# Kernel optimization log

Measured on AMD Instinct MI355X. Metric: run time of the kernel, lower is better.

The kernel has to match this reference:

```python
import jax, jax.numpy as jnp
import numpy as np

B, N, VD, AD, SD, HD = 32, 2048, 512, 128, 128, 64

def _lin_params(key, out_d, in_d, scale=0.05):
    k1, k2 = jax.random.split(key)
    w = jax.random.normal(k1, (out_d, in_d), jnp.float32) * scale
    b = jax.random.normal(k2, (out_d,), jnp.float32) * scale
    return w, b

def setup_inputs() -> dict:
    key = jax.random.key(0)
    ks = jax.random.split(key, 10)
    inp = {
        'vfeat': jax.random.normal(ks[0], (B, N, VD), jnp.float32),
        'afeat': jax.random.normal(ks[1], (B, N, AD), jnp.float32),
    }
    inp['vfc_w'], inp['vfc_b'] = _lin_params(ks[2], SD, VD)
    inp['afc_w'], inp['afc_b'] = _lin_params(ks[3], SD, AD)
    inp['am_w'],  inp['am_b']  = _lin_params(ks[4], SD, SD)
    inp['U_w'],   inp['U_b']   = _lin_params(ks[5], HD, SD)
    inp['V_w'],   inp['V_b']   = _lin_params(ks[6], HD, SD)
    inp['W_w'],   inp['W_b']   = _lin_params(ks[7], 1, HD)
    inp['cls_w'], inp['cls_b'] = _lin_params(ks[8], 2, SD)
    return inp

def reference(vfeat, afeat, vfc_w, vfc_b, afc_w, afc_b, am_w, am_b,
              U_w, U_b, V_w, V_b, W_w, W_b, cls_w, cls_b):
    # eval mode: dropout = identity, no softmax on scores
    vo1 = jax.nn.relu(jnp.einsum('bnd,kd->bnk', vfeat, vfc_w) + vfc_b)   # [B,N,128]
    ax = jax.nn.relu(jnp.einsum('bnd,kd->bnk', afeat, afc_w) + afc_b)    # [B,N,128]
    # AM (gated cross-modal attention): attfeat = vo1 * sigmoid(Linear(ax))
    gate = jax.nn.sigmoid(jnp.einsum('bnk,jk->bnj', ax, am_w) + am_b)
    ffeat = vo1 * gate + vo1                                             # attfeat + vo1
    # gated attention score head
    v = jax.nn.relu(jnp.einsum('bnk,hk->bnh', ffeat, V_w) + V_b)
    u = jax.nn.sigmoid(jnp.einsum('bnk,hk->bnh', ffeat, U_w) + U_b)
    scores = jnp.einsum('bnh,oh->bno', v * u, W_w) + W_b                 # [B,N,1]
    s = scores[..., 0]                                                   # [B,N]
    # attention-weighted pooling (batched mm replaces per-sample loop)
    zfeat = jnp.einsum('bn,bnk->bk', s, ffeat)                           # [B,128]
    logits = jnp.einsum('bk,ck->bc', zfeat, cls_w) + cls_b               # [B,2]
    return (s, logits)
```

## Files before the change

kernel.cpp:

```cpp
#include <hip/hip_runtime.h>
#include <hip/hip_bf16.h>

#define B_   32
#define N_   2048
#define VD_  512
#define AD_  128
#define SD_  128
#define TM   128
#define THREADS 512

typedef __attribute__((ext_vector_type(8))) short short8;
typedef __attribute__((ext_vector_type(4))) float f32x4;

__device__ __forceinline__ float sigmoidf_(float x) { return 1.0f / (1.0f + __expf(-x)); }

__device__ __forceinline__ ushort f2bf(float x) {
    union { float f; unsigned int i; } v; v.f = x;
    unsigned int r = v.i + 0x7FFFu + ((v.i >> 16) & 1u);
    return (ushort)(r >> 16);
}
__device__ __forceinline__ float bf2f(ushort u) {
    union { unsigned int i; float f; } v; v.i = ((unsigned int)u) << 16; return v.f;
}

__device__ __forceinline__ int swz(int row, int k, int ldk) {
    return row * ldk + (k ^ ((row & 7) << 3));
}

__device__ __forceinline__ void gemm_chunk(const ushort* Ab, int ldkA, int kA0,
                                           const ushort* Wb,
                                           int wr, int wc, int t16, int g4,
                                           f32x4 (&acc)[2][4])
{
    #pragma unroll
    for (int kk = 0; kk < 2; ++kk) {
        const int k = kk * 32 + g4 * 8;
        short8 a0 = *(const short8*)&Ab[swz(32 * wr + t16,      kA0 + k, ldkA)];
        short8 a1 = *(const short8*)&Ab[swz(32 * wr + 16 + t16, kA0 + k, ldkA)];
        #pragma unroll
        for (int n = 0; n < 4; ++n) {
            short8 bf = *(const short8*)&Wb[swz(64 * wc + 16 * n + t16, k, 64)];
            acc[0][n] = __builtin_amdgcn_mfma_f32_16x16x32_bf16(a0, bf, acc[0][n], 0, 0, 0);
            acc[1][n] = __builtin_amdgcn_mfma_f32_16x16x32_bf16(a1, bf, acc[1][n], 0, 0, 0);
        }
    }
}

__global__ __launch_bounds__(THREADS, 1)
void fused_mil(const float* __restrict__ vfeat, const float* __restrict__ afeat,
               const float* __restrict__ vfc_w, const float* __restrict__ vfc_b,
               const float* __restrict__ afc_w, const float* __restrict__ afc_b,
               const float* __restrict__ am_w,  const float* __restrict__ am_b,
               const float* __restrict__ U_w,   const float* __restrict__ U_b,
               const float* __restrict__ V_w,   const float* __restrict__ V_b,
               const float* __restrict__ W_w,   const float* __restrict__ W_b,
               float* __restrict__ s_out, float* __restrict__ zpart)
{
    __shared__ __align__(16) ushort Xbuf[128 * 128];
    __shared__ __align__(16) ushort Axb [128 * 128];
    __shared__ __align__(16) ushort Wb  [128 * 64];
    __shared__ __align__(16) ushort Cb  [128 * 64];
    __shared__ float sP[2][128];
    __shared__ float sS[128];
    __shared__ float zq[4][128];

    const int tid  = threadIdx.x;
    const int bx   = blockIdx.x;
    const int b    = bx >> 4;
    const int tok0 = (bx & 15) * TM;
    const int wid  = tid >> 6;
    const int lane = tid & 63;
    const int t16  = lane & 15;
    const int g4   = lane >> 4;
    const int wr   = wid >> 1;
    const int wc   = wid & 1;

    f32x4 acc[2][4], gacc[2][4];

    {
        const float4* src = (const float4*)(afeat + ((size_t)b * N_ + tok0) * AD_);
        #pragma unroll
        for (int i = 0; i < 8; ++i) {
            int fid = tid + i * THREADS;
            int r = fid >> 5, kq = fid & 31;
            float4 v = src[r * 32 + kq];
            ushort4 o; o.x = f2bf(v.x); o.y = f2bf(v.y); o.z = f2bf(v.z); o.w = f2bf(v.w);
            *(ushort4*)&Xbuf[swz(r, kq * 4, 128)] = o;
        }
    }

    #pragma unroll
    for (int m = 0; m < 2; ++m)
        #pragma unroll
        for (int n = 0; n < 4; ++n) acc[m][n] = (f32x4)0.0f;

    for (int kc = 0; kc < AD_; kc += 64) {
        #pragma unroll
        for (int i = 0; i < 4; ++i) {
            int fid = tid + i * THREADS;
            int c = fid >> 4, kq = fid & 15;
            float4 v = ((const float4*)afc_w)[c * 32 + (kc >> 2) + kq];
            ushort4 o; o.x = f2bf(v.x); o.y = f2bf(v.y); o.z = f2bf(v.z); o.w = f2bf(v.w);
            *(ushort4*)&Wb[swz(c, kq * 4, 64)] = o;
        }
        __syncthreads();
        gemm_chunk(Xbuf, 128, kc, Wb, wr, wc, t16, g4, acc);
        __syncthreads();
    }
    #pragma unroll
    for (int n = 0; n < 4; ++n) {
        int c = 64 * wc + 16 * n + t16;
        float bias = afc_b[c];
        #pragma unroll
        for (int m = 0; m < 2; ++m)
            #pragma unroll
            for (int r = 0; r < 4; ++r) {
                int row = 32 * wr + 16 * m + 4 * g4 + r;
                Axb[swz(row, c, 128)] = f2bf(fmaxf(acc[m][n][r] + bias, 0.0f));
            }
    }

    #pragma unroll
    for (int m = 0; m < 2; ++m)
        #pragma unroll
        for (int n = 0; n < 4; ++n) gacc[m][n] = (f32x4)0.0f;

    for (int kc = 0; kc < SD_; kc += 64) {
        #pragma unroll
        for (int i = 0; i < 4; ++i) {
            int fid = tid + i * THREADS;
            int c = fid >> 4, kq = fid & 15;
            float4 v = ((const float4*)am_w)[c * 32 + (kc >> 2) + kq];
            ushort4 o; o.x = f2bf(v.x); o.y = f2bf(v.y); o.z = f2bf(v.z); o.w = f2bf(v.w);
            *(ushort4*)&Wb[swz(c, kq * 4, 64)] = o;
        }
        __syncthreads();
        gemm_chunk(Axb, 128, kc, Wb, wr, wc, t16, g4, gacc);
        __syncthreads();
    }

    #pragma unroll
    for (int m = 0; m < 2; ++m)
        #pragma unroll
        for (int n = 0; n < 4; ++n) acc[m][n] = (f32x4)0.0f;

    {
        const float4* vsrc = (const float4*)(vfeat + ((size_t)b * N_ + tok0) * VD_);
        const float4* wsrc = (const float4*)vfc_w;
        float4 pv[4], pw[4];
        #pragma unroll
        for (int i = 0; i < 4; ++i) {
            int fid = tid + i * THREADS;
            int r = fid >> 4, kq = fid & 15;
            pv[i] = vsrc[r * 128 + kq];
            pw[i] = wsrc[r * 128 + kq];
        }
        for (int c = 0; c < 8; ++c) {
            #pragma unroll
            for (int i = 0; i < 4; ++i) {
                int fid = tid + i * THREADS;
                int r = fid >> 4, kq = fid & 15;
                ushort4 ov; ov.x = f2bf(pv[i].x); ov.y = f2bf(pv[i].y); ov.z = f2bf(pv[i].z); ov.w = f2bf(pv[i].w);
                *(ushort4*)&Cb[swz(r, kq * 4, 64)] = ov;
                ushort4 ow; ow.x = f2bf(pw[i].x); ow.y = f2bf(pw[i].y); ow.z = f2bf(pw[i].z); ow.w = f2bf(pw[i].w);
                *(ushort4*)&Wb[swz(r, kq * 4, 64)] = ow;
            }
            __syncthreads();
            if (c < 7) {
                int kq0 = (c + 1) * 16;
                #pragma unroll
                for (int i = 0; i < 4; ++i) {
                    int fid = tid + i * THREADS;
                    int r = fid >> 4, kq = fid & 15;
                    pv[i] = vsrc[r * 128 + kq0 + kq];
                    pw[i] = wsrc[r * 128 + kq0 + kq];
                }
            }
            gemm_chunk(Cb, 64, 0, Wb, wr, wc, t16, g4, acc);
            __syncthreads();
        }
    }

    #pragma unroll
    for (int n = 0; n < 4; ++n) {
        int c = 64 * wc + 16 * n + t16;
        float vb = vfc_b[c], ab = am_b[c];
        #pragma unroll
        for (int m = 0; m < 2; ++m)
            #pragma unroll
            for (int r = 0; r < 4; ++r) {
                int row = 32 * wr + 16 * m + 4 * g4 + r;
                float vo1 = fmaxf(acc[m][n][r] + vb, 0.0f);
                float g   = sigmoidf_(gacc[m][n][r] + ab);
                Xbuf[swz(row, c, 128)] = f2bf(vo1 * (1.0f + g));
            }
    }

    #pragma unroll
    for (int m = 0; m < 2; ++m)
        #pragma unroll
        for (int n = 0; n < 4; ++n) acc[m][n] = (f32x4)0.0f;

    for (int kc = 0; kc < SD_; kc += 64) {
        #pragma unroll
        for (int i = 0; i < 4; ++i) {
            int fid = tid + i * THREADS;
            int cc = fid >> 4, kq = fid & 15;
            int g = cc >> 5, q = cc & 31;
            int h = 32 * (g >> 1) + q;
            const float* srcrow = (g & 1) ? (U_w + (size_t)h * SD_) : (V_w + (size_t)h * SD_);
            float4 v = ((const float4*)srcrow)[(kc >> 2) + kq];
            ushort4 o; o.x = f2bf(v.x); o.y = f2bf(v.y); o.z = f2bf(v.z); o.w = f2bf(v.w);
            *(ushort4*)&Wb[swz(cc, kq * 4, 64)] = o;
        }
        __syncthreads();
        gemm_chunk(Xbuf, 128, kc, Wb, wr, wc, t16, g4, acc);
        __syncthreads();
    }

    #pragma unroll
    for (int m = 0; m < 2; ++m)
        #pragma unroll
        for (int r = 0; r < 4; ++r) {
            float p = 0.0f;
            #pragma unroll
            for (int n = 0; n < 2; ++n) {
                int h = 32 * wc + 16 * n + t16;
                float vv = fmaxf(acc[m][n][r] + V_b[h], 0.0f);
                float uu = sigmoidf_(acc[m][n + 2][r] + U_b[h]);
                p = fmaf(vv * uu, W_w[h], p);
            }
            p += __shfl_xor(p, 1);
            p += __shfl_xor(p, 2);
            p += __shfl_xor(p, 4);
            p += __shfl_xor(p, 8);
            if (t16 == 0) sP[wc][32 * wr + 16 * m + 4 * g4 + r] = p;
        }
    __syncthreads();
    if (tid < 128) {
        float s = sP[0][tid] + sP[1][tid] + W_b[0];
        sS[tid] = s;
        s_out[(size_t)b * N_ + tok0 + tid] = s;
    }
    __syncthreads();

    {
        int k = tid & 127, q = tid >> 7;
        float z = 0.0f;
        #pragma unroll
        for (int t = 0; t < 32; ++t) {
            int row = q * 32 + t;
            z = fmaf(sS[row], bf2f(Xbuf[swz(row, k, 128)]), z);
        }
        zq[q][k] = z;
    }
    __syncthreads();
    if (tid < 128)
        zpart[(size_t)bx * 128 + tid] = zq[0][tid] + zq[1][tid] + zq[2][tid] + zq[3][tid];
}

__global__ __launch_bounds__(128)
void reduce_logits(const float* __restrict__ zpart,
                   const float* __restrict__ cls_w, const float* __restrict__ cls_b,
                   float* __restrict__ out)
{
    __shared__ float sZ[128];
    int b = blockIdx.x, k = threadIdx.x;
    float z = 0.0f;
    #pragma unroll
    for (int t = 0; t < 16; ++t) z += zpart[(size_t)(b * 16 + t) * 128 + k];
    sZ[k] = z;
    __syncthreads();
    if (k < 2) {
        float acc = cls_b[k];
        for (int i = 0; i < 128; ++i) acc = fmaf(sZ[i], cls_w[k * 128 + i], acc);
        out[(size_t)B_ * N_ + b * 2 + k] = acc;
    }
}

extern "C" void kernel_launch(void* const* d_in, const int* in_sizes, int n_in,
                              void* d_out, int out_size, void* d_ws, size_t ws_size,
                              hipStream_t stream) {
    const float* vfeat = (const float*)d_in[0];
    const float* afeat = (const float*)d_in[1];
    const float* vfc_w = (const float*)d_in[2];
    const float* vfc_b = (const float*)d_in[3];
    const float* afc_w = (const float*)d_in[4];
    const float* afc_b = (const float*)d_in[5];
    const float* am_w  = (const float*)d_in[6];
    const float* am_b  = (const float*)d_in[7];
    const float* U_w   = (const float*)d_in[8];
    const float* U_b   = (const float*)d_in[9];
    const float* V_w   = (const float*)d_in[10];
    const float* V_b   = (const float*)d_in[11];
    const float* W_w   = (const float*)d_in[12];
    const float* W_b   = (const float*)d_in[13];
    const float* cls_w = (const float*)d_in[14];
    const float* cls_b = (const float*)d_in[15];

    float* out   = (float*)d_out;
    float* zpart = (float*)d_ws;

    fused_mil<<<dim3(B_ * 16), dim3(THREADS), 0, stream>>>(
        vfeat, afeat, vfc_w, vfc_b, afc_w, afc_b, am_w, am_b,
        U_w, U_b, V_w, V_b, W_w, W_b, out, zpart);
    reduce_logits<<<dim3(B_), dim3(128), 0, stream>>>(zpart, cls_w, cls_b, out);
}
```

Before: 60.34 us.

## Pre-convert weights to bf16 and read GEMM operands directly from global

Adds a small kernel that converts all weight matrices to bf16 once per call, stored in workspace. The main kernel then loads MFMA operands for the afeat and vfeat GEMMs directly from global memory, dropping the LDS staging buffers and most barriers. It also stores the gate in shared memory instead of registers and raises the occupancy hint to 4 blocks. The intent is to cut LDS traffic, barriers and repeated weight conversion and to allow more blocks per CU. In exchange, global loads are less coalesced and are not double-buffered, and the extra launch adds overhead.

```diff
diff --git a/kernel.cpp b/kernel.cpp
--- a/kernel.cpp
+++ b/kernel.cpp
@@ -12,6 +12,13 @@
 typedef __attribute__((ext_vector_type(8))) short short8;
 typedef __attribute__((ext_vector_type(4))) float f32x4;
 
+#define WOFF_VFC 0
+#define WOFF_AFC 65536
+#define WOFF_AM  81920
+#define WOFF_V   98304
+#define WOFF_U   106496
+#define WTOT     114688
+
 __device__ __forceinline__ float sigmoidf_(float x) { return 1.0f / (1.0f + __expf(-x)); }
 
 __device__ __forceinline__ ushort f2bf(float x) {
@@ -22,44 +29,85 @@
 __device__ __forceinline__ float bf2f(ushort u) {
     union { unsigned int i; float f; } v; v.i = ((unsigned int)u) << 16; return v.f;
 }
-
 __device__ __forceinline__ int swz(int row, int k, int ldk) {
     return row * ldk + (k ^ ((row & 7) << 3));
 }
-
-__device__ __forceinline__ void gemm_chunk(const ushort* Ab, int ldkA, int kA0,
-                                           const ushort* Wb,
-                                           int wr, int wc, int t16, int g4,
-                                           f32x4 (&acc)[2][4])
-{
-    #pragma unroll
-    for (int kk = 0; kk < 2; ++kk) {
-        const int k = kk * 32 + g4 * 8;
-        short8 a0 = *(const short8*)&Ab[swz(32 * wr + t16,      kA0 + k, ldkA)];
-        short8 a1 = *(const short8*)&Ab[swz(32 * wr + 16 + t16, kA0 + k, ldkA)];
+__device__ __forceinline__ short8 cvt8(const float* p) {
+    float4 x = ((const float4*)p)[0], y = ((const float4*)p)[1];
+    short8 r;
+    r[0] = (short)f2bf(x.x); r[1] = (short)f2bf(x.y); r[2] = (short)f2bf(x.z); r[3] = (short)f2bf(x.w);
+    r[4] = (short)f2bf(y.x); r[5] = (short)f2bf(y.y); r[6] = (short)f2bf(y.z); r[7] = (short)f2bf(y.w);
+    return r;
+}
+
+__global__ __launch_bounds__(256)
+void cvt_weights(const float* __restrict__ vfc, const float* __restrict__ afc,
+                 const float* __restrict__ am,  const float* __restrict__ Vw,
+                 const float* __restrict__ Uw,  ushort* __restrict__ dst)
+{
+    int e = (blockIdx.x * 256 + threadIdx.x) * 4;
+    if (e >= WTOT) return;
+    const float* src; int off;
+    if      (e < WOFF_AFC) { src = vfc; off = e - WOFF_VFC; }
+    else if (e < WOFF_AM)  { src = afc; off = e - WOFF_AFC; }
+    else if (e < WOFF_V)   { src = am;  off = e - WOFF_AM;  }
+    else if (e < WOFF_U)   { src = Vw;  off = e - WOFF_V;   }
+    else                   { src = Uw;  off = e - WOFF_U;   }
+    float4 v = *(const float4*)(src + off);
+    ushort4 o; o.x = f2bf(v.x); o.y = f2bf(v.y); o.z = f2bf(v.z); o.w = f2bf(v.w);
+    *(ushort4*)(dst + e) = o;
+}
+
+template<int K, int UNROLL>
+__device__ __forceinline__ void gemm_gf(const float* __restrict__ A,
+                                        const ushort* __restrict__ Bw,
+                                        int wr, int wc, int t16, int g4,
+                                        f32x4 (&acc)[2][4])
+{
+    #pragma unroll UNROLL
+    for (int ks = 0; ks < K; ks += 32) {
+        int k = ks + g4 * 8;
+        short8 a0 = cvt8(&A[(size_t)(32 * wr + t16) * K + k]);
+        short8 a1 = cvt8(&A[(size_t)(32 * wr + 16 + t16) * K + k]);
         #pragma unroll
         for (int n = 0; n < 4; ++n) {
-            short8 bf = *(const short8*)&Wb[swz(64 * wc + 16 * n + t16, k, 64)];
+            short8 bf = *(const short8*)&Bw[(64 * wc + 16 * n + t16) * K + k];
             acc[0][n] = __builtin_amdgcn_mfma_f32_16x16x32_bf16(a0, bf, acc[0][n], 0, 0, 0);
             acc[1][n] = __builtin_amdgcn_mfma_f32_16x16x32_bf16(a1, bf, acc[1][n], 0, 0, 0);
         }
     }
 }
 
-__global__ __launch_bounds__(THREADS, 1)
+template<int K>
+__device__ __forceinline__ void gemm_lf(const ushort* __restrict__ Ab,
+                                        const ushort* __restrict__ Bw,
+                                        int wr, int wc, int t16, int g4,
+                                        f32x4 (&acc)[2][4])
+{
+    #pragma unroll
+    for (int ks = 0; ks < K; ks += 32) {
+        int k = ks + g4 * 8;
+        short8 a0 = *(const short8*)&Ab[swz(32 * wr + t16,      k, 128)];
+        short8 a1 = *(const short8*)&Ab[swz(32 * wr + 16 + t16, k, 128)];
+        #pragma unroll
+        for (int n = 0; n < 4; ++n) {
+            short8 bf = *(const short8*)&Bw[(64 * wc + 16 * n + t16) * K + k];
+            acc[0][n] = __builtin_amdgcn_mfma_f32_16x16x32_bf16(a0, bf, acc[0][n], 0, 0, 0);
+            acc[1][n] = __builtin_amdgcn_mfma_f32_16x16x32_bf16(a1, bf, acc[1][n], 0, 0, 0);
+        }
+    }
+}
+
+__global__ __launch_bounds__(THREADS, 4)
 void fused_mil(const float* __restrict__ vfeat, const float* __restrict__ afeat,
-               const float* __restrict__ vfc_w, const float* __restrict__ vfc_b,
-               const float* __restrict__ afc_w, const float* __restrict__ afc_b,
-               const float* __restrict__ am_w,  const float* __restrict__ am_b,
-               const float* __restrict__ U_w,   const float* __restrict__ U_b,
-               const float* __restrict__ V_w,   const float* __restrict__ V_b,
+               const ushort* __restrict__ wsW,
+               const float* __restrict__ afc_b, const float* __restrict__ am_b,
+               const float* __restrict__ vfc_b,
+               const float* __restrict__ V_b,   const float* __restrict__ U_b,
                const float* __restrict__ W_w,   const float* __restrict__ W_b,
                float* __restrict__ s_out, float* __restrict__ zpart)
 {
     __shared__ __align__(16) ushort Xbuf[128 * 128];
-    __shared__ __align__(16) ushort Axb [128 * 128];
-    __shared__ __align__(16) ushort Wb  [128 * 64];
-    __shared__ __align__(16) ushort Cb  [128 * 64];
     __shared__ float sP[2][128];
     __shared__ float sS[128];
     __shared__ float zq[4][128];
@@ -75,38 +123,13 @@
     const int wr   = wid >> 1;
     const int wc   = wid & 1;
 
-    f32x4 acc[2][4], gacc[2][4];
-
-    {
-        const float4* src = (const float4*)(afeat + ((size_t)b * N_ + tok0) * AD_);
-        #pragma unroll
-        for (int i = 0; i < 8; ++i) {
-            int fid = tid + i * THREADS;
-            int r = fid >> 5, kq = fid & 31;
-            float4 v = src[r * 32 + kq];
-            ushort4 o; o.x = f2bf(v.x); o.y = f2bf(v.y); o.z = f2bf(v.z); o.w = f2bf(v.w);
-            *(ushort4*)&Xbuf[swz(r, kq * 4, 128)] = o;
-        }
-    }
+    f32x4 acc[2][4];
 
     #pragma unroll
     for (int m = 0; m < 2; ++m)
         #pragma unroll
         for (int n = 0; n < 4; ++n) acc[m][n] = (f32x4)0.0f;
-
-    for (int kc = 0; kc < AD_; kc += 64) {
-        #pragma unroll
-        for (int i = 0; i < 4; ++i) {
-            int fid = tid + i * THREADS;
-            int c = fid >> 4, kq = fid & 15;
-            float4 v = ((const float4*)afc_w)[c * 32 + (kc >> 2) + kq];
-            ushort4 o; o.x = f2bf(v.x); o.y = f2bf(v.y); o.z = f2bf(v.z); o.w = f2bf(v.w);
-            *(ushort4*)&Wb[swz(c, kq * 4, 64)] = o;
-        }
-        __syncthreads();
-        gemm_chunk(Xbuf, 128, kc, Wb, wr, wc, t16, g4, acc);
-        __syncthreads();
-    }
+    gemm_gf<AD_, 4>(afeat + ((size_t)b * N_ + tok0) * AD_, wsW + WOFF_AFC, wr, wc, t16, g4, acc);
     #pragma unroll
     for (int n = 0; n < 4; ++n) {
         int c = 64 * wc + 16 * n + t16;
@@ -116,106 +139,75 @@
             #pragma unroll
             for (int r = 0; r < 4; ++r) {
                 int row = 32 * wr + 16 * m + 4 * g4 + r;
-                Axb[swz(row, c, 128)] = f2bf(fmaxf(acc[m][n][r] + bias, 0.0f));
-            }
-    }
-
-    #pragma unroll
-    for (int m = 0; m < 2; ++m)
-        #pragma unroll
-        for (int n = 0; n < 4; ++n) gacc[m][n] = (f32x4)0.0f;
-
-    for (int kc = 0; kc < SD_; kc += 64) {
-        #pragma unroll
-        for (int i = 0; i < 4; ++i) {
-            int fid = tid + i * THREADS;
-            int c = fid >> 4, kq = fid & 15;
-            float4 v = ((const float4*)am_w)[c * 32 + (kc >> 2) + kq];
-            ushort4 o; o.x = f2bf(v.x); o.y = f2bf(v.y); o.z = f2bf(v.z); o.w = f2bf(v.w);
-            *(ushort4*)&Wb[swz(c, kq * 4, 64)] = o;
-        }
-        __syncthreads();
-        gemm_chunk(Axb, 128, kc, Wb, wr, wc, t16, g4, gacc);
-        __syncthreads();
-    }
+                Xbuf[swz(row, c, 128)] = f2bf(fmaxf(acc[m][n][r] + bias, 0.0f));
+            }
+    }
+    __syncthreads();
 
     #pragma unroll
     for (int m = 0; m < 2; ++m)
         #pragma unroll
         for (int n = 0; n < 4; ++n) acc[m][n] = (f32x4)0.0f;
-
-    {
-        const float4* vsrc = (const float4*)(vfeat + ((size_t)b * N_ + tok0) * VD_);
-        const float4* wsrc = (const float4*)vfc_w;
-        float4 pv[4], pw[4];
-        #pragma unroll
-        for (int i = 0; i < 4; ++i) {
-            int fid = tid + i * THREADS;
-            int r = fid >> 4, kq = fid & 15;
-            pv[i] = vsrc[r * 128 + kq];
-            pw[i] = wsrc[r * 128 + kq];
-        }
-        for (int c = 0; c < 8; ++c) {
-            #pragma unroll
-            for (int i = 0; i < 4; ++i) {
-                int fid = tid + i * THREADS;
-                int r = fid >> 4, kq = fid & 15;
-                ushort4 ov; ov.x = f2bf(pv[i].x); ov.y = f2bf(pv[i].y); ov.z = f2bf(pv[i].z); ov.w = f2bf(pv[i].w);
-                *(ushort4*)&Cb[swz(r, kq * 4, 64)] = ov;
-                ushort4 ow; ow.x = f2bf(pw[i].x); ow.y = f2bf(pw[i].y); ow.z = f2bf(pw[i].z); ow.w = f2bf(pw[i].w);
-                *(ushort4*)&Wb[swz(r, kq * 4, 64)] = ow;
-            }
-            __syncthreads();
-            if (c < 7) {
-                int kq0 = (c + 1) * 16;
-                #pragma unroll
-                for (int i = 0; i < 4; ++i) {
-                    int fid = tid + i * THREADS;
-                    int r = fid >> 4, kq = fid & 15;
-                    pv[i] = vsrc[r * 128 + kq0 + kq];
-                    pw[i] = wsrc[r * 128 + kq0 + kq];
-                }
-            }
-            gemm_chunk(Cb, 64, 0, Wb, wr, wc, t16, g4, acc);
-            __syncthreads();
-        }
-    }
-
+    gemm_lf<SD_>(Xbuf, wsW + WOFF_AM, wr, wc, t16, g4, acc);
+    __syncthreads();
     #pragma unroll
     for (int n = 0; n < 4; ++n) {
         int c = 64 * wc + 16 * n + t16;
-        float vb = vfc_b[c], ab = am_b[c];
+        float bias = am_b[c];
         #pragma unroll
         for (int m = 0; m < 2; ++m)
             #pragma unroll
             for (int r = 0; r < 4; ++r) {
                 int row = 32 * wr + 16 * m + 4 * g4 + r;
+                Xbuf[swz(row, c, 128)] = f2bf(sigmoidf_(acc[m][n][r] + bias));
+            }
+    }
+
+    #pragma unroll
+    for (int m = 0; m < 2; ++m)
+        #pragma unroll
+        for (int n = 0; n < 4; ++n) acc[m][n] = (f32x4)0.0f;
+    gemm_gf<VD_, 4>(vfeat + ((size_t)b * N_ + tok0) * VD_, wsW + WOFF_VFC, wr, wc, t16, g4, acc);
+
+    #pragma unroll
+    for (int n = 0; n < 4; ++n) {
+        int c = 64 * wc + 16 * n + t16;
+        float vb = vfc_b[c];
+        #pragma unroll
+        for (int m = 0; m < 2; ++m)
+            #pragma unroll
+            for (int r = 0; r < 4; ++r) {
+                int row = 32 * wr + 16 * m + 4 * g4 + r;
+                float g   = bf2f(Xbuf[swz(row, c, 128)]);
                 float vo1 = fmaxf(acc[m][n][r] + vb, 0.0f);
-                float g   = sigmoidf_(gacc[m][n][r] + ab);
                 Xbuf[swz(row, c, 128)] = f2bf(vo1 * (1.0f + g));
             }
     }
+    __syncthreads();
 
     #pragma unroll
     for (int m = 0; m < 2; ++m)
         #pragma unroll
         for (int n = 0; n < 4; ++n) acc[m][n] = (f32x4)0.0f;
-
-    for (int kc = 0; kc < SD_; kc += 64) {
-        #pragma unroll
-        for (int i = 0; i < 4; ++i) {
-            int fid = tid + i * THREADS;
-            int cc = fid >> 4, kq = fid & 15;
-            int g = cc >> 5, q = cc & 31;
-            int h = 32 * (g >> 1) + q;
-            const float* srcrow = (g & 1) ? (U_w + (size_t)h * SD_) : (V_w + (size_t)h * SD_);
-            float4 v = ((const float4*)srcrow)[(kc >> 2) + kq];
-            ushort4 o; o.x = f2bf(v.x); o.y = f2bf(v.y); o.z = f2bf(v.z); o.w = f2bf(v.w);
-            *(ushort4*)&Wb[swz(cc, kq * 4, 64)] = o;
-        }
-        __syncthreads();
-        gemm_chunk(Xbuf, 128, kc, Wb, wr, wc, t16, g4, acc);
-        __syncthreads();
+    {
+        const ushort* Vw = wsW + WOFF_V;
+        const ushort* Uw = wsW + WOFF_U;
+        #pragma unroll
+        for (int ks = 0; ks < SD_; ks += 32) {
+            int k = ks + g4 * 8;
+            short8 a0 = *(const short8*)&Xbuf[swz(32 * wr + t16,      k, 128)];
+            short8 a1 = *(const short8*)&Xbuf[swz(32 * wr + 16 + t16, k, 128)];
+            #pragma unroll
+            for (int n = 0; n < 2; ++n) {
+                int h = 32 * wc + 16 * n + t16;
+                short8 bv = *(const short8*)&Vw[h * SD_ + k];
+                short8 bu = *(const short8*)&Uw[h * SD_ + k];
+                acc[0][n]     = __builtin_amdgcn_mfma_f32_16x16x32_bf16(a0, bv, acc[0][n],     0, 0, 0);
+                acc[1][n]     = __builtin_amdgcn_mfma_f32_16x16x32_bf16(a1, bv, acc[1][n],     0, 0, 0);
+                acc[0][n + 2] = __builtin_amdgcn_mfma_f32_16x16x32_bf16(a0, bu, acc[0][n + 2], 0, 0, 0);
+                acc[1][n + 2] = __builtin_amdgcn_mfma_f32_16x16x32_bf16(a1, bu, acc[1][n + 2], 0, 0, 0);
+            }
+        }
     }
 
     #pragma unroll
@@ -299,10 +291,11 @@
     const float* cls_b = (const float*)d_in[15];
 
     float* out   = (float*)d_out;
-    float* zpart = (float*)d_ws;
-
+    ushort* wsW  = (ushort*)d_ws;
+    float* zpart = (float*)((char*)d_ws + (size_t)WTOT * 2);
+
+    cvt_weights<<<dim3(WTOT / 1024), dim3(256), 0, stream>>>(vfc_w, afc_w, am_w, V_w, U_w, wsW);
     fused_mil<<<dim3(B_ * 16), dim3(THREADS), 0, stream>>>(
-        vfeat, afeat, vfc_w, vfc_b, afc_w, afc_b, am_w, am_b,
-        U_w, U_b, V_w, V_b, W_w, W_b, out, zpart);
+        vfeat, afeat, wsW, afc_b, am_b, vfc_b, V_b, U_b, W_w, W_b, out, zpart);
     reduce_logits<<<dim3(B_), dim3(128), 0, stream>>>(zpart, cls_w, cls_b, out);
 }
```

Measured after the change: 108.1 us. 1.79x slower.
